# Performance work log

Measured on AMD Instinct MI355X. Metric: run time of the kernel, lower is better.

## Reference

```python
import jax, jax.numpy as jnp
import numpy as np

NUM_HEADS = 8
KEY_DIM = 16
VALUE_DIM = 16
MODES = (16, 16, 16)   # frequency modes kept per spatial dim (low + high corners)
PATCH = (4, 4, 4)      # frequency-domain patch grouping


def dht3(x):
    """3D discrete Hartley transform over the last three axes: real(FFT) - imag(FFT)."""
    X = jnp.fft.fftn(x.astype(jnp.complex64), axes=(-3, -2, -1))
    return X.real - X.imag


def _corner_idx(size, m):
    # low frequencies live at both ends of the FFT axis
    return jnp.concatenate([jnp.arange(m), jnp.arange(size - m, size)])


def truncate_modes(x, modes):
    """Keep the 8 low-frequency corners -> contiguous (2m0, 2m1, 2m2) block."""
    m0, m1, m2 = modes
    i0 = _corner_idx(x.shape[-3], m0)
    i1 = _corner_idx(x.shape[-2], m1)
    i2 = _corner_idx(x.shape[-1], m2)
    return x[..., i0[:, None, None], i1[None, :, None], i2[None, None, :]]


def grouping3d(x, patch):
    # x: (B, C, Z, D, H, W) -> (B, C*pd*ph*pw, Z, D//pd, H//ph, W//pw)
    pd, ph, pw = patch
    b, c, z, d, h, w = x.shape
    x = x.reshape(b, c, z, d // pd, pd, h // ph, ph, w // pw, pw)
    x = x.transpose(0, 1, 4, 6, 8, 2, 3, 5, 7)
    return x.reshape(b, c * pd * ph * pw, z, d // pd, h // ph, w // pw)


def ungrouping3d(x, c, patch):
    # inverse of grouping3d
    pd, ph, pw = patch
    b, _, z, nd, nh, nw = x.shape
    x = x.reshape(b, c, pd, ph, pw, z, nd, nh, nw)
    x = x.transpose(0, 1, 5, 6, 2, 7, 3, 8, 4)
    return x.reshape(b, c, z, nd * pd, nh * ph, nw * pw)


def setup_inputs() -> dict:
    key = jax.random.key(0)
    ks = jax.random.split(key, 5)
    B, D, H, W, C = 2, 64, 64, 64, 64
    x = jax.random.normal(ks[0], (B, D, H, W, C), jnp.float32)
    Wq = jax.random.normal(ks[1], (C, KEY_DIM, NUM_HEADS), jnp.float32) * 0.05
    Wk = jax.random.normal(ks[2], (C, KEY_DIM, NUM_HEADS), jnp.float32) * 0.05
    Wv = jax.random.normal(ks[3], (C, VALUE_DIM, NUM_HEADS), jnp.float32) * 0.05
    Wo = jax.random.normal(ks[4], (VALUE_DIM * NUM_HEADS, VALUE_DIM), jnp.float32) * 0.05
    return {"x": x, "Wq": Wq, "Wk": Wk, "Wv": Wv, "Wo": Wo}


def reference(x, Wq, Wk, Wv, Wo):
    B, D, H, W, C = x.shape
    m0, m1, m2 = MODES
    # Hartley transform (channels-first spatial layout)
    xh = dht3(jnp.transpose(x, (0, 4, 1, 2, 3)))          # (B, C, D, H, W)
    # mode truncation commutes with the channel-wise projections -> truncate first
    xt = truncate_modes(xh, MODES)                        # (B, C, 2m0, 2m1, 2m2)
    q = jnp.einsum('bcdhw,ckn->bkndhw', xt, Wq)           # (B, key, heads, 2m...)
    k = jnp.einsum('bcdhw,ckn->bkndhw', xt, Wk)
    v = jnp.einsum('bcdhw,cvn->bvndhw', xt, Wv)
    qg = grouping3d(q, PATCH)                             # (B, key*P, heads, nd, nh, nw)
    kg = grouping3d(k, PATCH)
    vg = grouping3d(v, PATCH)
    Bq, Cq, Hn, nd, nh, nw = qg.shape
    L = nd * nh * nw                                      # frequency-patch tokens
    qf = qg.reshape(B, Cq, Hn, L)
    kf = kg.reshape(B, Cq, Hn, L)
    vf = vg.reshape(B, vg.shape[1], Hn, L)
    # softmax-free attention: activation applied directly on Q^T K
    attn = jax.nn.selu(jnp.einsum('bchq,bchk->bhqk', qf, kf))
    of = jnp.einsum('bhqk,bchk->bchq', attn, vf)          # (B, val*P, heads, L)
    og = of.reshape(B, vg.shape[1], Hn, nd, nh, nw)
    ot = ungrouping3d(og, VALUE_DIM, PATCH)               # (B, val, heads, 2m0, 2m1, 2m2)
    ot = ot.reshape(B, VALUE_DIM * NUM_HEADS, 2 * m0, 2 * m1, 2 * m2)
    op = jnp.einsum('bidhw,io->bodhw', ot, Wo)            # (B, val, 2m...)
    # scatter the truncated block back into a zero full-size spectrum
    i0 = _corner_idx(D, m0)
    i1 = _corner_idx(H, m1)
    i2 = _corner_idx(W, m2)
    full = jnp.zeros((B, VALUE_DIM, D, H, W), op.dtype).at[
        :, :, i0[:, None, None], i1[None, :, None], i2[None, None, :]].set(op)
    # inverse DHT = DHT / N
    y = dht3(full) / (D * H * W)
    return jnp.transpose(y, (0, 2, 3, 4, 1))              # (B, D, H, W, val)
```

## Files before the change

kernel.cpp:

```cpp
#include <hip/hip_runtime.h>
#include <math.h>


typedef _Float16 half8 __attribute__((ext_vector_type(8)));
typedef float f32x4 __attribute__((ext_vector_type(4)));

static __device__ __forceinline__ float selu_f(float v) {
    return 1.0507009873554805f * (v > 0.f ? v : 1.6732632423543772f * (expf(v) - 1.f));
}

__global__ __launch_bounds__(256) void k_tables(float2* __restrict__ tab) {
    const int t = threadIdx.x;
    for (int i = t; i < 2048; i += 256) {
        const int a = i >> 5, f = i & 31;
        const int k = (f < 16) ? f : f + 32;
        const float ang = (float)((k * a) & 63) * 0.09817477042468103f;
        float s, c;
        sincosf(ang, &s, &c);
        tab[i] = make_float2(c, s);
        tab[2048 + i] = make_float2(c + s, s - c);
        tab[4096 + (f << 6) + a] = make_float2(c, s);
        tab[6144 + (f << 6) + a] = make_float2(c + s, s - c);
    }
}

__global__ __launch_bounds__(256) void k_fwd_w(const float* __restrict__ x,
                                               const float2* __restrict__ twF,
                                               float* __restrict__ re1, float* __restrict__ im1) {
    __shared__ __attribute__((aligned(16))) float xs[64][64];
    __shared__ __attribute__((aligned(16))) float2 tw[64][32];
    const int blk = blockIdx.x;
    const int t = threadIdx.x;
    const float* xp = x + (size_t)blk * 4096;
    for (int i = t; i < 1024; i += 256)
        *(float4*)&xs[i >> 4][(i & 15) * 4] = *(const float4*)&xp[i * 4];
    for (int i = t; i < 2048; i += 256) ((float2*)tw)[i] = twF[i];
    __syncthreads();
    const int c0 = (t & 15) * 4;
    const int f = t >> 4;
    float ar0[4] = {}, ai0[4] = {}, ar1[4] = {}, ai1[4] = {};
    #pragma unroll 8
    for (int w = 0; w < 64; ++w) {
        const float4 xv = *(const float4*)&xs[w][c0];
        const float2 t0 = tw[w][f];
        const float2 t1 = tw[w][f + 16];
        const float xa[4] = {xv.x, xv.y, xv.z, xv.w};
        #pragma unroll
        for (int c = 0; c < 4; ++c) {
            ar0[c] = fmaf(xa[c], t0.x, ar0[c]);
            ai0[c] = fmaf(xa[c], -t0.y, ai0[c]);
            ar1[c] = fmaf(xa[c], t1.x, ar1[c]);
            ai1[c] = fmaf(xa[c], -t1.y, ai1[c]);
        }
    }
    const size_t base = (size_t)blk * 2048;
    float4 o;
    o.x=ar0[0]; o.y=ar0[1]; o.z=ar0[2]; o.w=ar0[3]; *(float4*)&re1[base + f*64 + c0] = o;
    o.x=ai0[0]; o.y=ai0[1]; o.z=ai0[2]; o.w=ai0[3]; *(float4*)&im1[base + f*64 + c0] = o;
    o.x=ar1[0]; o.y=ar1[1]; o.z=ar1[2]; o.w=ar1[3]; *(float4*)&re1[base + (f+16)*64 + c0] = o;
    o.x=ai1[0]; o.y=ai1[1]; o.z=ai1[2]; o.w=ai1[3]; *(float4*)&im1[base + (f+16)*64 + c0] = o;
}

__global__ __launch_bounds__(256) void k_fwd_h(const float* __restrict__ re1, const float* __restrict__ im1,
                                               const float2* __restrict__ twF,
                                               float* __restrict__ re2, float* __restrict__ im2) {
    __shared__ __attribute__((aligned(16))) float rs[64][64], is[64][64];
    __shared__ __attribute__((aligned(16))) float2 tw[64][32];
    const int blk = blockIdx.x;
    const int f2 = blk & 31, bd = blk >> 5;
    const int t = threadIdx.x;
    for (int i = t; i < 1024; i += 256) {
        const int h = i >> 4, c4 = (i & 15) * 4;
        const size_t src = ((size_t)(bd * 64 + h) * 32 + f2) * 64 + c4;
        *(float4*)&rs[h][c4] = *(const float4*)&re1[src];
        *(float4*)&is[h][c4] = *(const float4*)&im1[src];
    }
    for (int i = t; i < 2048; i += 256) ((float2*)tw)[i] = twF[i];
    __syncthreads();
    const int c0 = (t & 15) * 4;
    const int f = t >> 4;
    float ar0[4] = {}, ai0[4] = {}, ar1[4] = {}, ai1[4] = {};
    #pragma unroll 4
    for (int h = 0; h < 64; ++h) {
        const float4 rv4 = *(const float4*)&rs[h][c0];
        const float4 iv4 = *(const float4*)&is[h][c0];
        const float2 t0 = tw[h][f];
        const float2 t1 = tw[h][f + 16];
        const float ra[4] = {rv4.x, rv4.y, rv4.z, rv4.w};
        const float ia[4] = {iv4.x, iv4.y, iv4.z, iv4.w};
        #pragma unroll
        for (int c = 0; c < 4; ++c) {
            ar0[c] = fmaf(ra[c], t0.x, ar0[c]); ar0[c] = fmaf(ia[c], t0.y, ar0[c]);
            ai0[c] = fmaf(ia[c], t0.x, ai0[c]); ai0[c] = fmaf(ra[c], -t0.y, ai0[c]);
            ar1[c] = fmaf(ra[c], t1.x, ar1[c]); ar1[c] = fmaf(ia[c], t1.y, ar1[c]);
            ai1[c] = fmaf(ia[c], t1.x, ai1[c]); ai1[c] = fmaf(ra[c], -t1.y, ai1[c]);
        }
    }
    float4 o;
    size_t dst = ((size_t)(bd * 32 + f) * 32 + f2) * 64 + c0;
    o.x=ar0[0]; o.y=ar0[1]; o.z=ar0[2]; o.w=ar0[3]; *(float4*)&re2[dst] = o;
    o.x=ai0[0]; o.y=ai0[1]; o.z=ai0[2]; o.w=ai0[3]; *(float4*)&im2[dst] = o;
    dst = ((size_t)(bd * 32 + f + 16) * 32 + f2) * 64 + c0;
    o.x=ar1[0]; o.y=ar1[1]; o.z=ar1[2]; o.w=ar1[3]; *(float4*)&re2[dst] = o;
    o.x=ai1[0]; o.y=ai1[1]; o.z=ai1[2]; o.w=ai1[3]; *(float4*)&im2[dst] = o;
}

__global__ __launch_bounds__(256) void k_fwd_d(const float* __restrict__ re2, const float* __restrict__ im2,
                                               const float2* __restrict__ twFd,
                                               float* __restrict__ xt) {
    __shared__ __attribute__((aligned(16))) float rs[64][64], is[64][64];
    __shared__ __attribute__((aligned(16))) float2 tw[64][32];
    const int blk = blockIdx.x;
    const int f2 = blk & 31, f1 = (blk >> 5) & 31, b = blk >> 10;
    const int t = threadIdx.x;
    for (int i = t; i < 1024; i += 256) {
        const int d = i >> 4, c4 = (i & 15) * 4;
        const size_t src = (((size_t)(b * 64 + d) * 32 + f1) * 32 + f2) * 64 + c4;
        *(float4*)&rs[d][c4] = *(const float4*)&re2[src];
        *(float4*)&is[d][c4] = *(const float4*)&im2[src];
    }
    for (int i = t; i < 2048; i += 256) ((float2*)tw)[i] = twFd[i];
    __syncthreads();
    const int c0 = (t & 15) * 4;
    const int f = t >> 4;
    float a0[4] = {}, a1[4] = {};
    #pragma unroll 4
    for (int d = 0; d < 64; ++d) {
        const float4 rv4 = *(const float4*)&rs[d][c0];
        const float4 iv4 = *(const float4*)&is[d][c0];
        const float2 p0 = tw[d][f];
        const float2 p1 = tw[d][f + 16];
        const float ra[4] = {rv4.x, rv4.y, rv4.z, rv4.w};
        const float ia[4] = {iv4.x, iv4.y, iv4.z, iv4.w};
        #pragma unroll
        for (int c = 0; c < 4; ++c) {
            a0[c] = fmaf(ra[c], p0.x, a0[c]); a0[c] = fmaf(ia[c], p0.y, a0[c]);
            a1[c] = fmaf(ra[c], p1.x, a1[c]); a1[c] = fmaf(ia[c], p1.y, a1[c]);
        }
    }
    float4 o;
    size_t dst = (((size_t)(b * 32 + f) * 32 + f1) * 32 + f2) * 64 + c0;
    o.x=a0[0]; o.y=a0[1]; o.z=a0[2]; o.w=a0[3]; *(float4*)&xt[dst] = o;
    dst = (((size_t)(b * 32 + f + 16) * 32 + f1) * 32 + f2) * 64 + c0;
    o.x=a1[0]; o.y=a1[1]; o.z=a1[2]; o.w=a1[3]; *(float4*)&xt[dst] = o;
}

__global__ __launch_bounds__(128) void k_qkv(const float* __restrict__ xt,
                                             const float* __restrict__ Wq, const float* __restrict__ Wk,
                                             const float* __restrict__ Wv,
                                             _Float16* __restrict__ Qh, _Float16* __restrict__ Kh,
                                             _Float16* __restrict__ Vh) {
    __shared__ float xs[64][65];
    const int blk = blockIdx.x;
    const int l = blk & 511, b = blk >> 9;
    const int nw = l & 7, nh = (l >> 3) & 7, nd = l >> 6;
    const int t = threadIdx.x;
    for (int i = t; i < 4096; i += 128) {
        const int pofs = i >> 6, c = i & 63;
        const int f0 = nd * 4 + (pofs >> 4);
        const int f1 = nh * 4 + ((pofs >> 2) & 3);
        const int f2 = nw * 4 + (pofs & 3);
        xs[pofs][c] = xt[((((size_t)b * 32 + f0) * 32 + f1) * 32 + f2) * 64 + c];
    }
    __syncthreads();
    const int kn = t;
    const int key = kn >> 3, n = kn & 7;
    #pragma unroll 1
    for (int p0 = 0; p0 < 64; p0 += 16) {
        float accq[16], acck[16], accv[16];
        #pragma unroll
        for (int i = 0; i < 16; ++i) { accq[i] = 0.f; acck[i] = 0.f; accv[i] = 0.f; }
        #pragma unroll 1
        for (int c0 = 0; c0 < 64; c0 += 16) {
            float wq[16], wk[16], wv[16];
            #pragma unroll
            for (int c = 0; c < 16; ++c) {
                wq[c] = Wq[(c0 + c) * 128 + kn];
                wk[c] = Wk[(c0 + c) * 128 + kn];
                wv[c] = Wv[(c0 + c) * 128 + kn];
            }
            #pragma unroll
            for (int p = 0; p < 16; ++p) {
                #pragma unroll
                for (int c = 0; c < 16; ++c) {
                    const float xv = xs[p0 + p][c0 + c];
                    accq[p] = fmaf(xv, wq[c], accq[p]);
                    acck[p] = fmaf(xv, wk[c], acck[p]);
                    accv[p] = fmaf(xv, wv[c], accv[p]);
                }
            }
        }
        const size_t base = (((size_t)(b * 8 + n) * 512 + l) * 1024 + key * 64 + p0);
        #pragma unroll
        for (int p = 0; p < 16; ++p) {
            Qh[base + p] = (_Float16)accq[p];
            Kh[base + p] = (_Float16)acck[p];
            Vh[base + p] = (_Float16)accv[p];
        }
    }
}

__global__ __launch_bounds__(256) void k_vt(const _Float16* __restrict__ Vh, _Float16* __restrict__ Vt) {
    __shared__ __attribute__((aligned(16))) _Float16 ldsT[64][72];
    const int blk = blockIdx.x;
    const int lt = blk & 7, rt = (blk >> 3) & 15, bh = blk >> 7;
    const int l0 = lt * 64, r0 = rt * 64;
    const int t = threadIdx.x;
    const int o8 = t & 7, li = t >> 3;
    const _Float16* src = Vh + (size_t)bh * 512 * 1024;
    _Float16* dst = Vt + (size_t)bh * 1024 * 512;
    #pragma unroll
    for (int p = 0; p < 2; ++p) {
        const int lr = li + p * 32;
        half8 v = *(const half8*)&src[(size_t)(l0 + lr) * 1024 + r0 + o8 * 8];
        #pragma unroll
        for (int jj = 0; jj < 8; ++jj) ldsT[o8 * 8 + jj][lr] = v[jj];
    }
    __syncthreads();
    #pragma unroll
    for (int p = 0; p < 2; ++p) {
        const int rr = li + p * 32;
        half8 v = *(const half8*)&ldsT[rr][o8 * 8];
        *(half8*)&dst[(size_t)(r0 + rr) * 512 + l0 + o8 * 8] = v;
    }
}

template<int KTOT, int NTOT, bool DOSELU, typename CT>
__global__ __launch_bounds__(256) void k_gemm(const _Float16* __restrict__ Ag,
                                              const _Float16* __restrict__ Bg,
                                              CT* __restrict__ Cg, float oscale) {
    __shared__ __attribute__((aligned(16))) _Float16 As[128 * 64];
    __shared__ __attribute__((aligned(16))) _Float16 Bs[128 * 64];
    const int bh = blockIdx.z;
    const int m0 = blockIdx.y * 128, n0 = blockIdx.x * 128;
    const _Float16* Ab = Ag + (size_t)bh * 512 * KTOT;
    const _Float16* Bb = Bg + (size_t)bh * NTOT * KTOT;
    CT* Cb = Cg + (size_t)bh * 512 * NTOT;
    const int t = threadIdx.x;
    const int o8 = t & 7, rstg = t >> 3;
    const int wv = t >> 6, l = t & 63, lr = l & 15, lk = l >> 4;
    const int wm = (wv >> 1) * 64, wn = (wv & 1) * 64;
    f32x4 acc[4][4];
    #pragma unroll
    for (int i = 0; i < 4; ++i)
        #pragma unroll
        for (int j = 0; j < 4; ++j) acc[i][j] = (f32x4){0.f, 0.f, 0.f, 0.f};
    #pragma unroll 1
    for (int k0 = 0; k0 < KTOT; k0 += 64) {
        if (k0) __syncthreads();
        #pragma unroll
        for (int p = 0; p < 4; ++p) {
            const int row = rstg + 32 * p;
            half8 va = *(const half8*)&Ab[(size_t)(m0 + row) * KTOT + k0 + o8 * 8];
            half8 vb = *(const half8*)&Bb[(size_t)(n0 + row) * KTOT + k0 + o8 * 8];
            const int by = (row * 128 + o8 * 16) ^ ((row & 7) << 4);
            *(half8*)((char*)As + by) = va;
            *(half8*)((char*)Bs + by) = vb;
        }
        __syncthreads();
        #pragma unroll
        for (int ks = 0; ks < 2; ++ks) {
            half8 af[4], bf[4];
            #pragma unroll
            for (int i = 0; i < 4; ++i) {
                const int ra = wm + i * 16 + lr;
                af[i] = *(const half8*)((const char*)As +
                        ((ra * 128 + ks * 64 + lk * 16) ^ ((ra & 7) << 4)));
                const int rb = wn + i * 16 + lr;
                bf[i] = *(const half8*)((const char*)Bs +
                        ((rb * 128 + ks * 64 + lk * 16) ^ ((rb & 7) << 4)));
            }
            #pragma unroll
            for (int i = 0; i < 4; ++i)
                #pragma unroll
                for (int j = 0; j < 4; ++j)
                    acc[i][j] = __builtin_amdgcn_mfma_f32_16x16x32_f16(af[i], bf[j], acc[i][j], 0, 0, 0);
        }
    }
    #pragma unroll
    for (int i = 0; i < 4; ++i) {
        #pragma unroll
        for (int r = 0; r < 4; ++r) {
            const int grow = m0 + wm + i * 16 + lk * 4 + r;
            #pragma unroll
            for (int j = 0; j < 4; ++j) {
                float v = acc[i][j][r];
                if (DOSELU) v = selu_f(v);
                v *= oscale;
                Cb[(size_t)grow * NTOT + n0 + wn + j * 16 + lr] = (CT)v;
            }
        }
    }
}

__global__ __launch_bounds__(256) void k_oproj(const float* __restrict__ Ob,
                                               const float* __restrict__ Wo,
                                               float* __restrict__ op) {
    __shared__ float Os[8][1024];
    __shared__ float Ws[2048];
    const int blk = blockIdx.x;
    const int l = blk & 511, b = blk >> 9;
    const int t = threadIdx.x;
    for (int i = t; i < 8192; i += 256) {
        const int h = i >> 10, r = i & 1023;
        Os[h][r] = Ob[((size_t)(b * 8 + h) * 512 + l) * 1024 + r];
    }
    for (int i = t; i < 2048; i += 256) Ws[i] = Wo[i];
    __syncthreads();
    const int pofs = t >> 2, o0 = (t & 3) * 4;
    float acc[4] = {0.f, 0.f, 0.f, 0.f};
    #pragma unroll
    for (int h = 0; h < 8; ++h) {
        #pragma unroll
        for (int val = 0; val < 16; ++val) {
            const float ov = Os[h][val * 64 + pofs];
            const int wi = (val * 8 + h) * 16;
            #pragma unroll
            for (int j = 0; j < 4; ++j) acc[j] = fmaf(ov, Ws[wi + o0 + j], acc[j]);
        }
    }
    const int nw = l & 7, nh = (l >> 3) & 7, nd = l >> 6;
    const int f0 = nd * 4 + (pofs >> 4);
    const int f1 = nh * 4 + ((pofs >> 2) & 3);
    const int f2 = nw * 4 + (pofs & 3);
    const size_t base = ((((size_t)b * 32 + f0) * 32 + f1) * 32 + f2) * 16 + o0;
    op[base + 0] = acc[0]; op[base + 1] = acc[1]; op[base + 2] = acc[2]; op[base + 3] = acc[3];
}

__global__ __launch_bounds__(256) void k_inv_d(const float* __restrict__ op,
                                               const float2* __restrict__ twI,
                                               float* __restrict__ ire, float* __restrict__ iim) {
    __shared__ __attribute__((aligned(16))) float s4[32][16];
    __shared__ __attribute__((aligned(16))) float2 tw[32][64];
    const int blk = blockIdx.x;
    const int k2 = blk & 31, k1 = (blk >> 5) & 31, b = blk >> 10;
    const int t = threadIdx.x;
    for (int i = t; i < 512; i += 256)
        s4[i >> 4][i & 15] = op[((size_t)(b * 32 + (i >> 4)) * 1024 + k1 * 32 + k2) * 16 + (i & 15)];
    for (int i = t; i < 2048; i += 256) ((float2*)tw)[i] = twI[i];
    __syncthreads();
    const int oq = (t & 3) * 4, d = t >> 2;
    float ar[4] = {}, ai[4] = {};
    #pragma unroll 8
    for (int r = 0; r < 32; ++r) {
        const float4 v4 = *(const float4*)&s4[r][oq];
        const float2 w = tw[r][d];
        const float va[4] = {v4.x, v4.y, v4.z, v4.w};
        #pragma unroll
        for (int c = 0; c < 4; ++c) {
            ar[c] = fmaf(va[c], w.x, ar[c]);
            ai[c] = fmaf(va[c], -w.y, ai[c]);
        }
    }
    const size_t dst = ((size_t)(b * 64 + d) * 1024 + k1 * 32 + k2) * 16 + oq;
    float4 o;
    o.x=ar[0]; o.y=ar[1]; o.z=ar[2]; o.w=ar[3]; *(float4*)&ire[dst] = o;
    o.x=ai[0]; o.y=ai[1]; o.z=ai[2]; o.w=ai[3]; *(float4*)&iim[dst] = o;
}

__global__ __launch_bounds__(256) void k_inv_h(const float* __restrict__ ire, const float* __restrict__ iim,
                                               const float2* __restrict__ twI,
                                               float* __restrict__ ore, float* __restrict__ oim) {
    __shared__ __attribute__((aligned(16))) float sr[32][16], si[32][16];
    __shared__ __attribute__((aligned(16))) float2 tw[32][64];
    const int blk = blockIdx.x;
    const int k2 = blk & 31, d = (blk >> 5) & 63, b = blk >> 11;
    const int t = threadIdx.x;
    for (int i = t; i < 512; i += 256) {
        const size_t src = ((size_t)(b * 64 + d) * 1024 + (i >> 4) * 32 + k2) * 16 + (i & 15);
        sr[i >> 4][i & 15] = ire[src];
        si[i >> 4][i & 15] = iim[src];
    }
    for (int i = t; i < 2048; i += 256) ((float2*)tw)[i] = twI[i];
    __syncthreads();
    const int oq = (t & 3) * 4, h = t >> 2;
    float ar[4] = {}, ai[4] = {};
    #pragma unroll 8
    for (int r = 0; r < 32; ++r) {
        const float4 rv4 = *(const float4*)&sr[r][oq];
        const float4 iv4 = *(const float4*)&si[r][oq];
        const float2 w = tw[r][h];
        const float ra[4] = {rv4.x, rv4.y, rv4.z, rv4.w};
        const float ia[4] = {iv4.x, iv4.y, iv4.z, iv4.w};
        #pragma unroll
        for (int c = 0; c < 4; ++c) {
            ar[c] = fmaf(ra[c], w.x, ar[c]); ar[c] = fmaf(ia[c], w.y, ar[c]);
            ai[c] = fmaf(ia[c], w.x, ai[c]); ai[c] = fmaf(ra[c], -w.y, ai[c]);
        }
    }
    const size_t dst = (((size_t)(b * 64 + d) * 64 + h) * 32 + k2) * 16 + oq;
    float4 o;
    o.x=ar[0]; o.y=ar[1]; o.z=ar[2]; o.w=ar[3]; *(float4*)&ore[dst] = o;
    o.x=ai[0]; o.y=ai[1]; o.z=ai[2]; o.w=ai[3]; *(float4*)&oim[dst] = o;
}

__global__ __launch_bounds__(256) void k_inv_w(const float* __restrict__ ire, const float* __restrict__ iim,
                                               const float2* __restrict__ twIw,
                                               float* __restrict__ outp) {
    __shared__ __attribute__((aligned(16))) float sr[32][16], si[32][16];
    __shared__ __attribute__((aligned(16))) float2 tw[32][64];
    const int blk = blockIdx.x;
    const int t = threadIdx.x;
    for (int i = t; i < 512; i += 256) {
        const size_t src = (size_t)blk * 512 + i;
        sr[i >> 4][i & 15] = ire[src];
        si[i >> 4][i & 15] = iim[src];
    }
    for (int i = t; i < 2048; i += 256) ((float2*)tw)[i] = twIw[i];
    __syncthreads();
    const int oq = (t & 3) * 4, w = t >> 2;
    float a[4] = {};
    #pragma unroll 8
    for (int r = 0; r < 32; ++r) {
        const float4 rv4 = *(const float4*)&sr[r][oq];
        const float4 iv4 = *(const float4*)&si[r][oq];
        const float2 p = tw[r][w];
        const float ra[4] = {rv4.x, rv4.y, rv4.z, rv4.w};
        const float ia[4] = {iv4.x, iv4.y, iv4.z, iv4.w};
        #pragma unroll
        for (int c = 0; c < 4; ++c) {
            a[c] = fmaf(ra[c], p.x, a[c]);
            a[c] = fmaf(ia[c], p.y, a[c]);
        }
    }
    const float sc = 3.814697265625e-06f;
    float4 o;
    o.x=a[0]*sc; o.y=a[1]*sc; o.z=a[2]*sc; o.w=a[3]*sc;
    *(float4*)&outp[((size_t)blk * 64 + w) * 16 + oq] = o;
}

extern "C" void kernel_launch(void* const* d_in, const int* in_sizes, int n_in,
                              void* d_out, int out_size, void* d_ws, size_t ws_size,
                              hipStream_t stream) {
    const float* x  = (const float*)d_in[0];
    const float* Wq = (const float*)d_in[1];
    const float* Wk = (const float*)d_in[2];
    const float* Wv = (const float*)d_in[3];
    const float* Wo = (const float*)d_in[4];
    float* outp = (float*)d_out;
    float* ws = (float*)d_ws;

    float2* tabs = (float2*)ws;
    const float2* twF  = tabs;
    const float2* twFd = tabs + 2048;
    const float2* twI  = tabs + 4096;
    const float2* twIw = tabs + 6144;

    float* re1 = ws + 32768;
    float* im1 = ws + 16809984;
    float* re2 = ws + 33587200;
    float* im2 = ws + 41975808;
    float* xt  = ws + 32768;
    _Float16* Qh = (_Float16*)(ws + 4227072);
    _Float16* Kh = (_Float16*)(ws + 8421376);
    _Float16* Vh = (_Float16*)(ws + 12615680);
    _Float16* Vt = (_Float16*)(ws + 16809984);
    _Float16* P  = (_Float16*)(ws + 21004288);
    float* Ob  = ws + 23101440;
    float* op  = ws + 31490048;
    float* ire1 = ws + 32538624;
    float* iim1 = ws + 34635776;
    float* ire2 = ws + 36732928;
    float* iim2 = ws + 40927232;

    k_tables<<<1, 256, 0, stream>>>(tabs);
    k_fwd_w<<<8192, 256, 0, stream>>>(x, twF, re1, im1);
    k_fwd_h<<<4096, 256, 0, stream>>>(re1, im1, twF, re2, im2);
    k_fwd_d<<<2048, 256, 0, stream>>>(re2, im2, twFd, xt);
    k_qkv<<<1024, 128, 0, stream>>>(xt, Wq, Wk, Wv, Qh, Kh, Vh);
    k_vt<<<2048, 256, 0, stream>>>(Vh, Vt);
    k_gemm<1024, 512, true, _Float16><<<dim3(4, 4, 16), 256, 0, stream>>>(Qh, Kh, P, 0.00390625f);
    k_gemm<512, 1024, false, float><<<dim3(8, 4, 16), 256, 0, stream>>>(P, Vt, Ob, 256.0f);
    k_oproj<<<1024, 256, 0, stream>>>(Ob, Wo, op);
    k_inv_d<<<2048, 256, 0, stream>>>(op, twI, ire1, iim1);
    k_inv_h<<<4096, 256, 0, stream>>>(ire1, iim1, twI, ire2, iim2);
    k_inv_w<<<8192, 256, 0, stream>>>(ire2, iim2, twIw, outp);
}
```

Before: 535.2 us.

## Move forward DHT stages and QKV projection onto fp16 MFMA matrix cores

Recasts the three forward Hartley/DFT stages (W, H, D axes) as small fp16 GEMMs against precomputed twiddle matrices and runs them with MFMA 16x16x32 instructions. The QKV projection also becomes MFMA-based, using pre-transposed fp16 weights built in the table kernel. Intermediates are stored in fp16 instead of separate fp32 real/imag buffers, and the layouts are changed to fit. This cuts FMA-bound scalar work and memory traffic, at the cost of fp16 rounding in the transform intermediates and a reshuffled workspace that overlaps buffers.

Result: faster. 442.2 us (-17.4%).

```diff
diff --git a/kernel.cpp b/kernel.cpp
--- a/kernel.cpp
+++ b/kernel.cpp
@@ -9,195 +9,243 @@
     return 1.0507009873554805f * (v > 0.f ? v : 1.6732632423543772f * (expf(v) - 1.f));
 }
 
-__global__ __launch_bounds__(256) void k_tables(float2* __restrict__ tab) {
+__global__ __launch_bounds__(256) void k_tables(const float* __restrict__ Wq, const float* __restrict__ Wk,
+                                                const float* __restrict__ Wv,
+                                                _Float16* __restrict__ A1g, _Float16* __restrict__ A2p,
+                                                _Float16* __restrict__ A3p,
+                                                _Float16* __restrict__ WqT, _Float16* __restrict__ WkT,
+                                                _Float16* __restrict__ WvT,
+                                                float2* __restrict__ twI, float2* __restrict__ twIw) {
     const int t = threadIdx.x;
     for (int i = t; i < 2048; i += 256) {
-        const int a = i >> 5, f = i & 31;
+        const int f = i & 31, a = i >> 5;
         const int k = (f < 16) ? f : f + 32;
         const float ang = (float)((k * a) & 63) * 0.09817477042468103f;
         float s, c;
         sincosf(ang, &s, &c);
-        tab[i] = make_float2(c, s);
-        tab[2048 + i] = make_float2(c + s, s - c);
-        tab[4096 + (f << 6) + a] = make_float2(c, s);
-        tab[6144 + (f << 6) + a] = make_float2(c + s, s - c);
+        A1g[(2 * f + 0) * 64 + a] = (_Float16)c;
+        A1g[(2 * f + 1) * 64 + a] = (_Float16)(-s);
+        A2p[(2 * f + 0) * 128 + a]      = (_Float16)c;
+        A2p[(2 * f + 0) * 128 + 64 + a] = (_Float16)s;
+        A2p[(2 * f + 1) * 128 + a]      = (_Float16)(-s);
+        A2p[(2 * f + 1) * 128 + 64 + a] = (_Float16)c;
+        A3p[f * 128 + a]      = (_Float16)(c + s);
+        A3p[f * 128 + 64 + a] = (_Float16)(s - c);
+        twI[(f << 6) + a]  = make_float2(c, s);
+        twIw[(f << 6) + a] = make_float2(c + s, s - c);
+    }
+    for (int i = t; i < 8192; i += 256) {
+        const int kn = i >> 6, c = i & 63;
+        WqT[i] = (_Float16)Wq[c * 128 + kn];
+        WkT[i] = (_Float16)Wk[c * 128 + kn];
+        WvT[i] = (_Float16)Wv[c * 128 + kn];
     }
 }
 
 __global__ __launch_bounds__(256) void k_fwd_w(const float* __restrict__ x,
-                                               const float2* __restrict__ twF,
-                                               float* __restrict__ re1, float* __restrict__ im1) {
-    __shared__ __attribute__((aligned(16))) float xs[64][64];
-    __shared__ __attribute__((aligned(16))) float2 tw[64][32];
+                                               const _Float16* __restrict__ A1g,
+                                               _Float16* __restrict__ t1) {
+    __shared__ _Float16 X1[64][72];
     const int blk = blockIdx.x;
     const int t = threadIdx.x;
     const float* xp = x + (size_t)blk * 4096;
-    for (int i = t; i < 1024; i += 256)
-        *(float4*)&xs[i >> 4][(i & 15) * 4] = *(const float4*)&xp[i * 4];
-    for (int i = t; i < 2048; i += 256) ((float2*)tw)[i] = twF[i];
-    __syncthreads();
-    const int c0 = (t & 15) * 4;
-    const int f = t >> 4;
-    float ar0[4] = {}, ai0[4] = {}, ar1[4] = {}, ai1[4] = {};
-    #pragma unroll 8
-    for (int w = 0; w < 64; ++w) {
-        const float4 xv = *(const float4*)&xs[w][c0];
-        const float2 t0 = tw[w][f];
-        const float2 t1 = tw[w][f + 16];
-        const float xa[4] = {xv.x, xv.y, xv.z, xv.w};
-        #pragma unroll
-        for (int c = 0; c < 4; ++c) {
-            ar0[c] = fmaf(xa[c], t0.x, ar0[c]);
-            ai0[c] = fmaf(xa[c], -t0.y, ai0[c]);
-            ar1[c] = fmaf(xa[c], t1.x, ar1[c]);
-            ai1[c] = fmaf(xa[c], -t1.y, ai1[c]);
-        }
-    }
-    const size_t base = (size_t)blk * 2048;
-    float4 o;
-    o.x=ar0[0]; o.y=ar0[1]; o.z=ar0[2]; o.w=ar0[3]; *(float4*)&re1[base + f*64 + c0] = o;
-    o.x=ai0[0]; o.y=ai0[1]; o.z=ai0[2]; o.w=ai0[3]; *(float4*)&im1[base + f*64 + c0] = o;
-    o.x=ar1[0]; o.y=ar1[1]; o.z=ar1[2]; o.w=ar1[3]; *(float4*)&re1[base + (f+16)*64 + c0] = o;
-    o.x=ai1[0]; o.y=ai1[1]; o.z=ai1[2]; o.w=ai1[3]; *(float4*)&im1[base + (f+16)*64 + c0] = o;
-}
-
-__global__ __launch_bounds__(256) void k_fwd_h(const float* __restrict__ re1, const float* __restrict__ im1,
-                                               const float2* __restrict__ twF,
-                                               float* __restrict__ re2, float* __restrict__ im2) {
-    __shared__ __attribute__((aligned(16))) float rs[64][64], is[64][64];
-    __shared__ __attribute__((aligned(16))) float2 tw[64][32];
+    for (int i = t; i < 1024; i += 256) {
+        const float4 v = ((const float4*)xp)[i];
+        const int w = i >> 4, c0 = (i & 15) * 4;
+        X1[c0 + 0][w] = (_Float16)v.x;
+        X1[c0 + 1][w] = (_Float16)v.y;
+        X1[c0 + 2][w] = (_Float16)v.z;
+        X1[c0 + 3][w] = (_Float16)v.w;
+    }
+    __syncthreads();
+    const int wv = t >> 6, l = t & 63, lr = l & 15, lk = l >> 4;
+    const int mh = (wv >> 1) * 32, nh = (wv & 1) * 32;
+    half8 af[2][2], bf[2][2];
+    #pragma unroll
+    for (int i = 0; i < 2; ++i)
+        #pragma unroll
+        for (int ks = 0; ks < 2; ++ks) {
+            af[i][ks] = *(const half8*)&A1g[(mh + i * 16 + lr) * 64 + ks * 32 + lk * 8];
+            bf[i][ks] = *(const half8*)&X1[nh + i * 16 + lr][ks * 32 + lk * 8];
+        }
+    f32x4 acc[2][2];
+    #pragma unroll
+    for (int i = 0; i < 2; ++i)
+        #pragma unroll
+        for (int j = 0; j < 2; ++j) acc[i][j] = (f32x4){0.f, 0.f, 0.f, 0.f};
+    #pragma unroll
+    for (int ks = 0; ks < 2; ++ks)
+        #pragma unroll
+        for (int i = 0; i < 2; ++i)
+            #pragma unroll
+            for (int j = 0; j < 2; ++j)
+                acc[i][j] = __builtin_amdgcn_mfma_f32_16x16x32_f16(af[i][ks], bf[j][ks], acc[i][j], 0, 0, 0);
+    _Float16* op = t1 + (size_t)blk * 4096;
+    #pragma unroll
+    for (int i = 0; i < 2; ++i)
+        #pragma unroll
+        for (int j = 0; j < 2; ++j)
+            #pragma unroll
+            for (int r = 0; r < 4; ++r)
+                op[(mh + i * 16 + lk * 4 + r) * 64 + nh + j * 16 + lr] = (_Float16)acc[i][j][r];
+}
+
+__global__ __launch_bounds__(256) void k_fh(const _Float16* __restrict__ t1,
+                                            const _Float16* __restrict__ A2p,
+                                            _Float16* __restrict__ t2) {
+    __shared__ _Float16 X2[2][64][72];
     const int blk = blockIdx.x;
     const int f2 = blk & 31, bd = blk >> 5;
     const int t = threadIdx.x;
     for (int i = t; i < 1024; i += 256) {
-        const int h = i >> 4, c4 = (i & 15) * 4;
-        const size_t src = ((size_t)(bd * 64 + h) * 32 + f2) * 64 + c4;
-        *(float4*)&rs[h][c4] = *(const float4*)&re1[src];
-        *(float4*)&is[h][c4] = *(const float4*)&im1[src];
-    }
-    for (int i = t; i < 2048; i += 256) ((float2*)tw)[i] = twF[i];
-    __syncthreads();
-    const int c0 = (t & 15) * 4;
-    const int f = t >> 4;
-    float ar0[4] = {}, ai0[4] = {}, ar1[4] = {}, ai1[4] = {};
-    #pragma unroll 4
-    for (int h = 0; h < 64; ++h) {
-        const float4 rv4 = *(const float4*)&rs[h][c0];
-        const float4 iv4 = *(const float4*)&is[h][c0];
-        const float2 t0 = tw[h][f];
-        const float2 t1 = tw[h][f + 16];
-        const float ra[4] = {rv4.x, rv4.y, rv4.z, rv4.w};
-        const float ia[4] = {iv4.x, iv4.y, iv4.z, iv4.w};
-        #pragma unroll
-        for (int c = 0; c < 4; ++c) {
-            ar0[c] = fmaf(ra[c], t0.x, ar0[c]); ar0[c] = fmaf(ia[c], t0.y, ar0[c]);
-            ai0[c] = fmaf(ia[c], t0.x, ai0[c]); ai0[c] = fmaf(ra[c], -t0.y, ai0[c]);
-            ar1[c] = fmaf(ra[c], t1.x, ar1[c]); ar1[c] = fmaf(ia[c], t1.y, ar1[c]);
-            ai1[c] = fmaf(ia[c], t1.x, ai1[c]); ai1[c] = fmaf(ra[c], -t1.y, ai1[c]);
-        }
-    }
-    float4 o;
-    size_t dst = ((size_t)(bd * 32 + f) * 32 + f2) * 64 + c0;
-    o.x=ar0[0]; o.y=ar0[1]; o.z=ar0[2]; o.w=ar0[3]; *(float4*)&re2[dst] = o;
-    o.x=ai0[0]; o.y=ai0[1]; o.z=ai0[2]; o.w=ai0[3]; *(float4*)&im2[dst] = o;
-    dst = ((size_t)(bd * 32 + f + 16) * 32 + f2) * 64 + c0;
-    o.x=ar1[0]; o.y=ar1[1]; o.z=ar1[2]; o.w=ar1[3]; *(float4*)&re2[dst] = o;
-    o.x=ai1[0]; o.y=ai1[1]; o.z=ai1[2]; o.w=ai1[3]; *(float4*)&im2[dst] = o;
-}
-
-__global__ __launch_bounds__(256) void k_fwd_d(const float* __restrict__ re2, const float* __restrict__ im2,
-                                               const float2* __restrict__ twFd,
-                                               float* __restrict__ xt) {
-    __shared__ __attribute__((aligned(16))) float rs[64][64], is[64][64];
-    __shared__ __attribute__((aligned(16))) float2 tw[64][32];
+        const int h = i >> 4, q = i & 15;
+        const half8 v = *(const half8*)(t1 + ((size_t)(bd * 64 + h) << 12) + (f2 << 7) + (q << 3));
+        const int ri = q >> 3, c0 = (q & 7) * 8;
+        #pragma unroll
+        for (int j = 0; j < 8; ++j) X2[ri][c0 + j][h] = v[j];
+    }
+    __syncthreads();
+    const int wv = t >> 6, l = t & 63, lr = l & 15, lk = l >> 4;
+    const int mh = (wv >> 1) * 32, nh = (wv & 1) * 32;
+    half8 af[2][4], bf[2][4];
+    #pragma unroll
+    for (int i = 0; i < 2; ++i)
+        #pragma unroll
+        for (int ks = 0; ks < 4; ++ks) {
+            af[i][ks] = *(const half8*)&A2p[(mh + i * 16 + lr) * 128 + ks * 32 + lk * 8];
+            bf[i][ks] = *(const half8*)&X2[ks >> 1][nh + i * 16 + lr][(ks & 1) * 32 + lk * 8];
+        }
+    f32x4 acc[2][2];
+    #pragma unroll
+    for (int i = 0; i < 2; ++i)
+        #pragma unroll
+        for (int j = 0; j < 2; ++j) acc[i][j] = (f32x4){0.f, 0.f, 0.f, 0.f};
+    #pragma unroll
+    for (int ks = 0; ks < 4; ++ks)
+        #pragma unroll
+        for (int i = 0; i < 2; ++i)
+            #pragma unroll
+            for (int j = 0; j < 2; ++j)
+                acc[i][j] = __builtin_amdgcn_mfma_f32_16x16x32_f16(af[i][ks], bf[j][ks], acc[i][j], 0, 0, 0);
+    _Float16* op = t2 + ((size_t)(bd * 32 + f2) << 12);
+    #pragma unroll
+    for (int i = 0; i < 2; ++i)
+        #pragma unroll
+        for (int j = 0; j < 2; ++j)
+            #pragma unroll
+            for (int r = 0; r < 4; ++r)
+                op[(mh + i * 16 + lk * 4 + r) * 64 + nh + j * 16 + lr] = (_Float16)acc[i][j][r];
+}
+
+__global__ __launch_bounds__(256) void k_fd(const _Float16* __restrict__ t2,
+                                            const _Float16* __restrict__ A3p,
+                                            _Float16* __restrict__ xt) {
+    __shared__ _Float16 X3[2][64][72];
     const int blk = blockIdx.x;
     const int f2 = blk & 31, f1 = (blk >> 5) & 31, b = blk >> 10;
     const int t = threadIdx.x;
     for (int i = t; i < 1024; i += 256) {
-        const int d = i >> 4, c4 = (i & 15) * 4;
-        const size_t src = (((size_t)(b * 64 + d) * 32 + f1) * 32 + f2) * 64 + c4;
-        *(float4*)&rs[d][c4] = *(const float4*)&re2[src];
-        *(float4*)&is[d][c4] = *(const float4*)&im2[src];
-    }
-    for (int i = t; i < 2048; i += 256) ((float2*)tw)[i] = twFd[i];
-    __syncthreads();
-    const int c0 = (t & 15) * 4;
-    const int f = t >> 4;
-    float a0[4] = {}, a1[4] = {};
-    #pragma unroll 4
-    for (int d = 0; d < 64; ++d) {
-        const float4 rv4 = *(const float4*)&rs[d][c0];
-        const float4 iv4 = *(const float4*)&is[d][c0];
-        const float2 p0 = tw[d][f];
-        const float2 p1 = tw[d][f + 16];
-        const float ra[4] = {rv4.x, rv4.y, rv4.z, rv4.w};
-        const float ia[4] = {iv4.x, iv4.y, iv4.z, iv4.w};
-        #pragma unroll
-        for (int c = 0; c < 4; ++c) {
-            a0[c] = fmaf(ra[c], p0.x, a0[c]); a0[c] = fmaf(ia[c], p0.y, a0[c]);
-            a1[c] = fmaf(ra[c], p1.x, a1[c]); a1[c] = fmaf(ia[c], p1.y, a1[c]);
-        }
-    }
-    float4 o;
-    size_t dst = (((size_t)(b * 32 + f) * 32 + f1) * 32 + f2) * 64 + c0;
-    o.x=a0[0]; o.y=a0[1]; o.z=a0[2]; o.w=a0[3]; *(float4*)&xt[dst] = o;
-    dst = (((size_t)(b * 32 + f + 16) * 32 + f1) * 32 + f2) * 64 + c0;
-    o.x=a1[0]; o.y=a1[1]; o.z=a1[2]; o.w=a1[3]; *(float4*)&xt[dst] = o;
-}
-
-__global__ __launch_bounds__(128) void k_qkv(const float* __restrict__ xt,
-                                             const float* __restrict__ Wq, const float* __restrict__ Wk,
-                                             const float* __restrict__ Wv,
+        const int d = i >> 4, q = i & 15;
+        const half8 v = *(const half8*)(t2 + (((size_t)(b * 64 + d) * 32 + f2) << 12) + (f1 << 7) + (q << 3));
+        const int ri = q >> 3, c0 = (q & 7) * 8;
+        #pragma unroll
+        for (int j = 0; j < 8; ++j) X3[ri][c0 + j][d] = v[j];
+    }
+    __syncthreads();
+    const int wv = t >> 6, l = t & 63, lr = l & 15, lk = l >> 4;
+    const int it = wv >> 1, nh = (wv & 1) * 32;
+    half8 af[4], bf[2][4];
+    #pragma unroll
+    for (int ks = 0; ks < 4; ++ks) {
+        af[ks] = *(const half8*)&A3p[(it * 16 + lr) * 128 + ks * 32 + lk * 8];
+        #pragma unroll
+        for (int j = 0; j < 2; ++j)
+            bf[j][ks] = *(const half8*)&X3[ks >> 1][nh + j * 16 + lr][(ks & 1) * 32 + lk * 8];
+    }
+    f32x4 acc[2];
+    acc[0] = (f32x4){0.f, 0.f, 0.f, 0.f};
+    acc[1] = (f32x4){0.f, 0.f, 0.f, 0.f};
+    #pragma unroll
+    for (int ks = 0; ks < 4; ++ks)
+        #pragma unroll
+        for (int j = 0; j < 2; ++j)
+            acc[j] = __builtin_amdgcn_mfma_f32_16x16x32_f16(af[ks], bf[j][ks], acc[j], 0, 0, 0);
+    _Float16* op = xt + ((size_t)blk << 11);
+    #pragma unroll
+    for (int j = 0; j < 2; ++j)
+        #pragma unroll
+        for (int r = 0; r < 4; ++r)
+            op[(it * 16 + lk * 4 + r) * 64 + nh + j * 16 + lr] = (_Float16)acc[j][r];
+}
+
+__global__ __launch_bounds__(256) void k_qkv(const _Float16* __restrict__ xt,
+                                             const _Float16* __restrict__ WqT, const _Float16* __restrict__ WkT,
+                                             const _Float16* __restrict__ WvT,
                                              _Float16* __restrict__ Qh, _Float16* __restrict__ Kh,
                                              _Float16* __restrict__ Vh) {
-    __shared__ float xs[64][65];
-    const int blk = blockIdx.x;
-    const int l = blk & 511, b = blk >> 9;
-    const int nw = l & 7, nh = (l >> 3) & 7, nd = l >> 6;
-    const int t = threadIdx.x;
-    for (int i = t; i < 4096; i += 128) {
-        const int pofs = i >> 6, c = i & 63;
-        const int f0 = nd * 4 + (pofs >> 4);
-        const int f1 = nh * 4 + ((pofs >> 2) & 3);
-        const int f2 = nw * 4 + (pofs & 3);
-        xs[pofs][c] = xt[((((size_t)b * 32 + f0) * 32 + f1) * 32 + f2) * 64 + c];
-    }
-    __syncthreads();
-    const int kn = t;
-    const int key = kn >> 3, n = kn & 7;
-    #pragma unroll 1
-    for (int p0 = 0; p0 < 64; p0 += 16) {
-        float accq[16], acck[16], accv[16];
-        #pragma unroll
-        for (int i = 0; i < 16; ++i) { accq[i] = 0.f; acck[i] = 0.f; accv[i] = 0.f; }
-        #pragma unroll 1
-        for (int c0 = 0; c0 < 64; c0 += 16) {
-            float wq[16], wk[16], wv[16];
-            #pragma unroll
-            for (int c = 0; c < 16; ++c) {
-                wq[c] = Wq[(c0 + c) * 128 + kn];
-                wk[c] = Wk[(c0 + c) * 128 + kn];
-                wv[c] = Wv[(c0 + c) * 128 + kn];
-            }
-            #pragma unroll
-            for (int p = 0; p < 16; ++p) {
+    __shared__ _Float16 xs[64][72];
+    __shared__ _Float16 ldso[8][1024];
+    const int blk = blockIdx.x;
+    const int lI = blk & 511, b = blk >> 9;
+    const int tw_ = lI & 7, th_ = (lI >> 3) & 7, td_ = lI >> 6;
+    const int t = threadIdx.x;
+    for (int i = t; i < 512; i += 256) {
+        const int pofs = i >> 3, c0 = (i & 7) * 8;
+        const int f0 = td_ * 4 + (pofs >> 4);
+        const int f1 = th_ * 4 + ((pofs >> 2) & 3);
+        const int f2 = tw_ * 4 + (pofs & 3);
+        const half8 v = *(const half8*)(xt + ((((size_t)(b * 32 + f1) * 32 + f2) * 32 + f0) << 6) + c0);
+        *(half8*)&xs[pofs][c0] = v;
+    }
+    __syncthreads();
+    const int wv = t >> 6, l = t & 63, lr = l & 15, lk = l >> 4;
+    const int knb = wv * 32;
+    half8 af[4][2];
+    #pragma unroll
+    for (int i = 0; i < 4; ++i)
+        #pragma unroll
+        for (int ks = 0; ks < 2; ++ks)
+            af[i][ks] = *(const half8*)&xs[i * 16 + lr][ks * 32 + lk * 8];
+
+    auto do_mat = [&](const _Float16* __restrict__ WT, _Float16* __restrict__ dst) {
+        half8 bf[2][2];
+        #pragma unroll
+        for (int j = 0; j < 2; ++j)
+            #pragma unroll
+            for (int ks = 0; ks < 2; ++ks)
+                bf[j][ks] = *(const half8*)&WT[(knb + j * 16 + lr) * 64 + ks * 32 + lk * 8];
+        f32x4 acc[4][2];
+        #pragma unroll
+        for (int i = 0; i < 4; ++i)
+            #pragma unroll
+            for (int j = 0; j < 2; ++j) acc[i][j] = (f32x4){0.f, 0.f, 0.f, 0.f};
+        #pragma unroll
+        for (int ks = 0; ks < 2; ++ks)
+            #pragma unroll
+            for (int i = 0; i < 4; ++i)
                 #pragma unroll
-                for (int c = 0; c < 16; ++c) {
-                    const float xv = xs[p0 + p][c0 + c];
-                    accq[p] = fmaf(xv, wq[c], accq[p]);
-                    acck[p] = fmaf(xv, wk[c], acck[p]);
-                    accv[p] = fmaf(xv, wv[c], accv[p]);
+                for (int j = 0; j < 2; ++j)
+                    acc[i][j] = __builtin_amdgcn_mfma_f32_16x16x32_f16(af[i][ks], bf[j][ks], acc[i][j], 0, 0, 0);
+        #pragma unroll
+        for (int i = 0; i < 4; ++i)
+            #pragma unroll
+            for (int j = 0; j < 2; ++j)
+                #pragma unroll
+                for (int r = 0; r < 4; ++r) {
+                    const int p = i * 16 + lk * 4 + r;
+                    const int kn = knb + j * 16 + lr;
+                    ldso[kn & 7][p * 16 + (kn >> 3)] = (_Float16)acc[i][j][r];
                 }
-            }
-        }
-        const size_t base = (((size_t)(b * 8 + n) * 512 + l) * 1024 + key * 64 + p0);
-        #pragma unroll
-        for (int p = 0; p < 16; ++p) {
-            Qh[base + p] = (_Float16)accq[p];
-            Kh[base + p] = (_Float16)acck[p];
-            Vh[base + p] = (_Float16)accv[p];
-        }
-    }
+        __syncthreads();
+        for (int i = t; i < 1024; i += 256) {
+            const int n = i >> 7, o8 = (i & 127) * 8;
+            *(half8*)(dst + (((size_t)(b * 8 + n) * 512 + lI) << 10) + o8) = *(const half8*)&ldso[n][o8];
+        }
+        __syncthreads();
+    };
+    do_mat(WqT, Qh);
+    do_mat(WkT, Kh);
+    do_mat(WvT, Vh);
 }
 
 __global__ __launch_bounds__(256) void k_vt(const _Float16* __restrict__ Vh, _Float16* __restrict__ Vt) {
@@ -299,11 +347,11 @@
     __shared__ float Os[8][1024];
     __shared__ float Ws[2048];
     const int blk = blockIdx.x;
-    const int l = blk & 511, b = blk >> 9;
+    const int lI = blk & 511, b = blk >> 9;
     const int t = threadIdx.x;
     for (int i = t; i < 8192; i += 256) {
         const int h = i >> 10, r = i & 1023;
-        Os[h][r] = Ob[((size_t)(b * 8 + h) * 512 + l) * 1024 + r];
+        Os[h][r] = Ob[((size_t)(b * 8 + h) * 512 + lI) * 1024 + r];
     }
     for (int i = t; i < 2048; i += 256) Ws[i] = Wo[i];
     __syncthreads();
@@ -313,13 +361,13 @@
     for (int h = 0; h < 8; ++h) {
         #pragma unroll
         for (int val = 0; val < 16; ++val) {
-            const float ov = Os[h][val * 64 + pofs];
+            const float ov = Os[h][pofs * 16 + val];
             const int wi = (val * 8 + h) * 16;
             #pragma unroll
             for (int j = 0; j < 4; ++j) acc[j] = fmaf(ov, Ws[wi + o0 + j], acc[j]);
         }
     }
-    const int nw = l & 7, nh = (l >> 3) & 7, nd = l >> 6;
+    const int nw = lI & 7, nh = (lI >> 3) & 7, nd = lI >> 6;
     const int f0 = nd * 4 + (pofs >> 4);
     const int f1 = nh * 4 + ((pofs >> 2) & 3);
     const int f2 = nw * 4 + (pofs & 3);
@@ -440,34 +488,35 @@
     float* outp = (float*)d_out;
     float* ws = (float*)d_ws;
 
-    float2* tabs = (float2*)ws;
-    const float2* twF  = tabs;
-    const float2* twFd = tabs + 2048;
-    const float2* twI  = tabs + 4096;
-    const float2* twIw = tabs + 6144;
-
-    float* re1 = ws + 32768;
-    float* im1 = ws + 16809984;
-    float* re2 = ws + 33587200;
-    float* im2 = ws + 41975808;
-    float* xt  = ws + 32768;
-    _Float16* Qh = (_Float16*)(ws + 4227072);
-    _Float16* Kh = (_Float16*)(ws + 8421376);
-    _Float16* Vh = (_Float16*)(ws + 12615680);
-    _Float16* Vt = (_Float16*)(ws + 16809984);
-    _Float16* P  = (_Float16*)(ws + 21004288);
-    float* Ob  = ws + 23101440;
-    float* op  = ws + 31490048;
-    float* ire1 = ws + 32538624;
-    float* iim1 = ws + 34635776;
-    float* ire2 = ws + 36732928;
-    float* iim2 = ws + 40927232;
-
-    k_tables<<<1, 256, 0, stream>>>(tabs);
-    k_fwd_w<<<8192, 256, 0, stream>>>(x, twF, re1, im1);
-    k_fwd_h<<<4096, 256, 0, stream>>>(re1, im1, twF, re2, im2);
-    k_fwd_d<<<2048, 256, 0, stream>>>(re2, im2, twFd, xt);
-    k_qkv<<<1024, 128, 0, stream>>>(xt, Wq, Wk, Wv, Qh, Kh, Vh);
+    _Float16* A1g = (_Float16*)(ws + 0);
+    _Float16* A2p = (_Float16*)(ws + 2048);
+    _Float16* A3p = (_Float16*)(ws + 6144);
+    _Float16* WqT = (_Float16*)(ws + 8192);
+    _Float16* WkT = (_Float16*)(ws + 12288);
+    _Float16* WvT = (_Float16*)(ws + 16384);
+    float2* twI   = (float2*)(ws + 20480);
+    float2* twIw  = (float2*)(ws + 24576);
+
+    _Float16* t1 = (_Float16*)(ws + 32768);
+    _Float16* t2 = (_Float16*)(ws + 16809984);
+    _Float16* xt = (_Float16*)(ws + 25198592);
+    _Float16* Qh = (_Float16*)(ws + 27295744);
+    _Float16* Kh = (_Float16*)(ws + 31490048);
+    _Float16* Vh = (_Float16*)(ws + 35684352);
+    _Float16* Vt = (_Float16*)(ws + 39878656);
+    _Float16* P  = (_Float16*)(ws + 32768);
+    float* Ob    = ws + 16809984;
+    float* op    = ws + 27295744;
+    float* ire1  = ws + 31490048;
+    float* iim1  = ws + 33587200;
+    float* ire2  = ws + 35684352;
+    float* iim2  = ws + 39878656;
+
+    k_tables<<<1, 256, 0, stream>>>(Wq, Wk, Wv, A1g, A2p, A3p, WqT, WkT, WvT, twI, twIw);
+    k_fwd_w<<<8192, 256, 0, stream>>>(x, A1g, t1);
+    k_fh<<<4096, 256, 0, stream>>>(t1, A2p, t2);
+    k_fd<<<2048, 256, 0, stream>>>(t2, A3p, xt);
+    k_qkv<<<1024, 256, 0, stream>>>(xt, WqT, WkT, WvT, Qh, Kh, Vh);
     k_vt<<<2048, 256, 0, stream>>>(Vh, Vt);
     k_gemm<1024, 512, true, _Float16><<<dim3(4, 4, 16), 256, 0, stream>>>(Qh, Kh, P, 0.00390625f);
     k_gemm<512, 1024, false, float><<<dim3(8, 4, 16), 256, 0, stream>>>(P, Vt, Ob, 256.0f);
```
